# Performance work log

Hardware: AMD Instinct MI355X
Metric: run time of the kernel (lower is better)

The kernel has to match this reference:

```python
import jax, jax.numpy as jnp
import numpy as np

H, DK, NHID, L, G = 8, 32, 256, 2, 16
SQRT_DK = float(np.sqrt(DK))
N_IN = (3, 3, 2)  # number of etypes whose dst is word, topic, doc (for mean cross-reducer)


def _seg_softmax_agg(a, val, dst, n):
    # per-destination-node softmax over incoming edges (DGL mailbox softmax), then weighted sum
    m = jax.ops.segment_max(a, dst, num_segments=n)
    m = jnp.where(m < -1e30, 0.0, m)  # empty segments
    ex = jnp.exp(a - m[dst])
    den = jax.ops.segment_sum(ex, dst, num_segments=n)
    w = ex / jnp.maximum(den, 1e-9)[dst]
    return jax.ops.segment_sum(w[..., None] * val, dst, num_segments=n)  # [n,H,DK]


def _forward(word_id, topic_id, g_word, g_topic, g_doc,
             src_ww, dst_ww, src_wd, dst_wd, src_wt, dst_wt, src_td, dst_td, src_tt, dst_tt,
             time_ww, time_wd, time_wt, time_td, y_data,
             word_embeds, topic_embeds, doc_gen, adapt_w, adapt_b,
             time_tab, time_w, time_b,
             kW, kB, qW, qB, vW, vB, aW, aB, skip, ln_g, ln_b,
             pri, attR, msgR, out_w, out_b):
    nd = g_doc.shape[0]
    # initial node features: word via adapt_ws, topic lookup, doc broadcast
    h = [word_embeds[word_id] @ adapt_w + adapt_b,
         topic_embeds[topic_id],
         jnp.tile(doc_gen, (nd, 1))]
    te = lambda t: time_tab[t] @ time_w + time_b  # RelTemporalEncoding: lin(emb(t)) -> [E, DK]
    th_ww, th_wd, th_wt, th_td = te(time_ww), te(time_wd), te(time_wt), te(time_td)
    # etype index order: wt, wd, td, tt, ww, tw, dt, dw ; ntype index: 0=word,1=topic,2=doc
    rels = [(0, 0, 1, src_wt, dst_wt, th_wt), (1, 0, 2, src_wd, dst_wd, th_wd),
            (2, 1, 2, src_td, dst_td, th_td), (3, 1, 1, src_tt, dst_tt, None),
            (4, 0, 0, src_ww, dst_ww, th_ww), (5, 1, 0, dst_wt, src_wt, th_wt),
            (6, 2, 1, dst_td, src_td, th_td), (7, 2, 0, dst_wd, src_wd, th_wd)]
    for li in range(L):
        k = [(h[i] @ kW[li, i] + kB[li, i]).reshape(-1, H, DK) for i in range(3)]
        q = [(h[i] @ qW[li, i] + qB[li, i]).reshape(-1, H, DK) for i in range(3)]
        v = [(h[i] @ vW[li, i] + vB[li, i]).reshape(-1, H, DK) for i in range(3)]
        t = [jnp.zeros((h[i].shape[0], NHID), h[i].dtype) for i in range(3)]
        for (e, s, d, src, dst, th) in rels:
            key = jnp.einsum('ehk,hkl->ehl', k[s][src], attR[li, e])
            a = (q[d][dst] * key).sum(-1) * pri[li, e] / SQRT_DK  # [E,H]
            val = jnp.einsum('ehk,hkl->ehl', v[s][src], msgR[li, e])
            if th is not None:
                val = val + th[:, None, :]  # temporal encoding broadcast over heads
            n = h[d].shape[0]
            he = _seg_softmax_agg(a, val, dst, n)
            t[d] = t[d] + jax.nn.relu(he.reshape(n, NHID))  # relu per etype, then mean
        nh = []
        for i in range(3):
            alpha = jax.nn.sigmoid(skip[li, i])
            trans = (t[i] / N_IN[i]) @ aW[li, i] + aB[li, i]
            out = trans * alpha + h[i] * (1.0 - alpha)
            mu = out.mean(-1, keepdims=True)
            var = ((out - mu) ** 2).mean(-1, keepdims=True)
            nh.append((out - mu) / jnp.sqrt(var + 1e-5) * ln_g[li, i] + ln_b[li, i])
        h = nh
    gmax = lambda x, g: jax.ops.segment_max(x, g, num_segments=G)  # dgl.max_nodes
    gi = jnp.concatenate([gmax(h[2], g_doc), gmax(h[0], g_word), gmax(h[1], g_topic)], -1)
    logits = gi @ out_w + out_b  # [G,1]
    z = logits.reshape(-1)
    loss = jnp.mean(jnp.maximum(z, 0.0) - z * y_data + jnp.log1p(jnp.exp(-jnp.abs(z))))
    return loss, jax.nn.sigmoid(logits)


def setup_inputs():
    key = jax.random.key(0)
    ks = iter(jax.random.split(key, 80))
    nrm = lambda shape, s=0.05: jax.random.normal(next(ks), shape, jnp.float32) * s
    ri = lambda shape, hi: jax.random.randint(next(ks), shape, 0, hi)
    NW, NT, ND = 30000, 2000, 8000
    d = {}
    d['word_id'] = ri((NW,), 15000)
    d['topic_id'] = ri((NT,), 50)
    d['g_word'] = jnp.sort(ri((NW,), G))
    d['g_topic'] = jnp.sort(ri((NT,), G))
    d['g_doc'] = jnp.sort(ri((ND,), G))
    d['src_ww'] = ri((40000,), NW); d['dst_ww'] = ri((40000,), NW); d['time_ww'] = ri((40000,), 7)
    d['src_wd'] = ri((30000,), NW); d['dst_wd'] = ri((30000,), ND); d['time_wd'] = ri((30000,), 7)
    d['src_wt'] = ri((30000,), NW); d['dst_wt'] = ri((30000,), NT); d['time_wt'] = ri((30000,), 7)
    d['src_td'] = ri((25000,), NT); d['dst_td'] = ri((25000,), ND); d['time_td'] = ri((25000,), 7)
    d['src_tt'] = ri((20000,), NT); d['dst_tt'] = ri((20000,), NT)
    d['y_data'] = jax.random.uniform(next(ks), (G,), jnp.float32)
    d['word_embeds'] = nrm((15000, 256))
    d['topic_embeds'] = nrm((50, 256), 0.1)
    d['doc_gen'] = nrm((1, 256), 0.1)
    d['adapt_w'] = nrm((256, 256)); d['adapt_b'] = nrm((256,), 0.01)
    d['time_tab'] = nrm((7, 32), 0.1); d['time_w'] = nrm((32, 32), 0.1); d['time_b'] = nrm((32,), 0.01)
    for nm in ['kW', 'qW', 'vW', 'aW']:
        d[nm] = nrm((L, 3, 256, 256))
    for nm in ['kB', 'qB', 'vB', 'aB']:
        d[nm] = nrm((L, 3, 256), 0.01)
    d['skip'] = jnp.ones((L, 3))
    d['ln_g'] = jnp.ones((L, 3, 256)); d['ln_b'] = jnp.zeros((L, 3, 256))
    d['pri'] = jnp.ones((L, 8, H))
    d['attR'] = nrm((L, 8, H, DK, DK), 0.1)
    d['msgR'] = nrm((L, 8, H, DK, DK), 0.1)
    d['out_w'] = nrm((3 * NHID, 1)); d['out_b'] = jnp.zeros((1,))
    return d


def reference(word_id, topic_id, g_word, g_topic, g_doc,
              src_ww, dst_ww, time_ww, src_wd, dst_wd, time_wd,
              src_wt, dst_wt, time_wt, src_td, dst_td, time_td,
              src_tt, dst_tt, y_data,
              word_embeds, topic_embeds, doc_gen, adapt_w, adapt_b,
              time_tab, time_w, time_b,
              kW, kB, qW, qB, vW, vB, aW, aB, skip, ln_g, ln_b,
              pri, attR, msgR, out_w, out_b):
    return _forward(word_id, topic_id, g_word, g_topic, g_doc,
                    src_ww, dst_ww, src_wd, dst_wd, src_wt, dst_wt, src_td, dst_td, src_tt, dst_tt,
                    time_ww, time_wd, time_wt, time_td, y_data,
                    word_embeds, topic_embeds, doc_gen, adapt_w, adapt_b,
                    time_tab, time_w, time_b,
                    kW, kB, qW, qB, vW, vB, aW, aB, skip, ln_g, ln_b,
                    pri, attR, msgR, out_w, out_b)
```

## Files before the change

kernel.cpp:

```cpp
#include <hip/hip_runtime.h>
#include <hip/hip_bf16.h>
#include <math.h>

#define H 8
#define DK 32
#define NHID 256
#define LNUM 2
#define GNUM 16

typedef float f32x4 __attribute__((ext_vector_type(4)));
typedef short bf16x8 __attribute__((ext_vector_type(8)));
typedef unsigned short u16x8 __attribute__((ext_vector_type(8)));

__device__ __forceinline__ unsigned encf(float f) {
    unsigned u = __float_as_uint(f);
    return (u & 0x80000000u) ? ~u : (u | 0x80000000u);
}
__device__ __forceinline__ float decf(unsigned u) {
    return __uint_as_float((u & 0x80000000u) ? (u ^ 0x80000000u) : ~u);
}
__device__ __forceinline__ float bfd(unsigned short u) {
    return __uint_as_float(((unsigned)u) << 16);
}
__device__ __forceinline__ unsigned short f2bf(float x) {
    __hip_bfloat16 b = __float2bfloat16(x);
    return *reinterpret_cast<unsigned short*>(&b);
}

#define APAN2(row, kb) ((((kb) >> 7) << 12) + ((row) << 6) + ((((kb) & 127) ^ (((row) & 7) << 4)) >> 1))
__device__ __forceinline__ size_t swzA(int row, int col ) {
    return (((size_t)(row >> 6)) << 14) + (size_t)APAN2(row & 63, col * 2);
}
#define SWZB(row, kb)  (((row) << 6) + ((((kb) ^ (((row) & 7) << 4))) >> 1))

struct CsrArgs  { const int* dst[8]; int relOfs[9]; int dstBase[8]; };
struct BdAllArgs{ int rows[8]; int srcOfs[8]; int outOfs[8]; };
struct Ek1AllArgs{ const int* src[8]; const int* dst[8]; int E[8]; int eBase[8];
                   int kOfs[8]; int qOfs[8]; };
struct Ek3AllArgs{ const int* src[8]; const int* tim[8]; int eBase[8]; int dstBase[8];
                   int vOfs[8]; int typeRel[9]; int nrT[3]; int cumN[4]; int tOfs[3];
                   float oScale[3]; };
struct GmaxArgs { const float* hp[3]; const int* grp[3]; int n[3]; int colBase[3]; };
struct GBArgs   { int rb[4]; int nLoc[3]; int li3; };
struct MLArgs   { int rowOfs[4]; int nLoc[3]; int li3; };

__global__ void te_kernel(const float* __restrict__ time_tab, const float* __restrict__ time_w,
                          const float* __restrict__ time_b, float* __restrict__ te7) {
    int t = threadIdx.x >> 5, j = threadIdx.x & 31;
    if (t < 7) {
        float s = time_b[j];
        #pragma unroll
        for (int i = 0; i < 32; ++i) s += time_tab[t * 32 + i] * time_w[i * 32 + j];
        te7[t * 32 + j] = s;
    }
}

__global__ void gather_rows(const float* __restrict__ emb, const int* __restrict__ idx,
                            float* __restrict__ out, unsigned short* __restrict__ outB, int n) {
    int row = blockIdx.x, c = threadIdx.x;
    if (row < n) {
        float v = emb[(size_t)idx[row] * 256 + c];
        out[(size_t)row * 256 + c] = v;
        outB[swzA(row, c)] = f2bf(v);
    }
}

__global__ void bcast_row(const float* __restrict__ src, float* __restrict__ out,
                          unsigned short* __restrict__ outB, int n) {
    int row = blockIdx.x, c = threadIdx.x;
    if (row < n) {
        float v = src[c];
        out[(size_t)row * 256 + c] = v;
        outB[swzA(row, c)] = f2bf(v);
    }
}

__global__ __launch_bounds__(256) void wtr_kernel(
    const float* __restrict__ adaptW, const float* __restrict__ kW, const float* __restrict__ qW,
    const float* __restrict__ vW, const float* __restrict__ aW, unsigned short* __restrict__ WT) {
    int z = blockIdx.z;
    const float* src;
    if (z == 0) src = adaptW;
    else if (z < 7)  src = kW + (size_t)(z - 1) * 65536;
    else if (z < 13) src = qW + (size_t)(z - 7) * 65536;
    else if (z < 19) src = vW + (size_t)(z - 13) * 65536;
    else             src = aW + (size_t)(z - 19) * 65536;
    unsigned short* dst = WT + (size_t)z * 65536;
    __shared__ float tile[32][33];
    int tx = threadIdx.x & 31, ty = threadIdx.x >> 5;
    int kb = blockIdx.x * 32, cb = blockIdx.y * 32;
    #pragma unroll
    for (int i = 0; i < 4; ++i)
        tile[ty + i * 8][tx] = src[(size_t)(kb + ty + i * 8) * 256 + cb + tx];
    __syncthreads();
    #pragma unroll
    for (int i = 0; i < 4; ++i) {
        int col = cb + ty + i * 8, k = kb + tx;
        dst[((col >> 6) * 4 + (k >> 6)) * 4096 + SWZB(col & 63, (k & 63) * 2)] =
            f2bf(tile[tx][ty + i * 8]);
    }
}

__global__ __launch_bounds__(256) void gemm_batch(
    const unsigned short* __restrict__ Apan,
    const unsigned short* __restrict__ WT, int wBase, int nz,
    const float* __restrict__ b0, const float* __restrict__ b1, const float* __restrict__ b2,
    void* __restrict__ o0, void* __restrict__ o1, void* __restrict__ o2,
    int outBf16, GBArgs ga)
{
    __shared__ unsigned short As[64 * 256];
    __shared__ unsigned short Bs[2][4096];
    const int tid = threadIdx.x;
    const int lane = tid & 63, wv = tid >> 6;
    const int b = blockIdx.x;
    const int t = (b >= ga.rb[2]) ? 2 : ((b >= ga.rb[1]) ? 1 : 0);
    const int nLoc = ga.nLoc[t];
    const int locRowBase = (b - ga.rb[t]) * 64;
    const int cb6 = blockIdx.y;
    const int mBase = wBase + ga.li3 + t;
    {
        const u16x8* src = reinterpret_cast<const u16x8*>(Apan + (((size_t)b) << 14));
        u16x8* dst = reinterpret_cast<u16x8*>(As);
        #pragma unroll
        for (int it = 0; it < 8; ++it)
            dst[it * 256 + tid] = src[it * 256 + tid];
    }
    const int fr = lane & 15, fg = lane >> 4;
    const int wrow = (wv & 1) * 32, wcol = (wv >> 1) * 32;
    const int nt = nz * 4;
    {
        const u16x8* src = reinterpret_cast<const u16x8*>(WT + (size_t)mBase * 65536 + (size_t)(cb6 * 4 + 0) * 4096);
        u16x8* dst = reinterpret_cast<u16x8*>(Bs[0]);
        dst[tid] = src[tid];
        dst[tid + 256] = src[tid + 256];
    }
    __syncthreads();

    f32x4 acc[2][2];
    #pragma unroll
    for (int m = 0; m < 2; ++m)
        #pragma unroll
        for (int nn = 0; nn < 2; ++nn) acc[m][nn] = 0.f;

    for (int tt2 = 0; tt2 < nt; ++tt2) {
        const int cur = tt2 & 1;
        const int ks = tt2 & 3, z = tt2 >> 2;
        u16x8 w0, w1;
        const bool pf = (tt2 + 1 < nt);
        if (pf) {
            int tn = tt2 + 1;
            const u16x8* src = reinterpret_cast<const u16x8*>(
                WT + (size_t)(mBase + (tn >> 2) * 6) * 65536 + (size_t)(cb6 * 4 + (tn & 3)) * 4096);
            w0 = src[tid];
            w1 = src[tid + 256];
        }
        #pragma unroll
        for (int kk = 0; kk < 2; ++kk) {
            bf16x8 af0 = *reinterpret_cast<bf16x8*>(&As[APAN2(wrow + fr,      ks * 128 + kk * 64 + fg * 16)]);
            bf16x8 af1 = *reinterpret_cast<bf16x8*>(&As[APAN2(wrow + 16 + fr, ks * 128 + kk * 64 + fg * 16)]);
            bf16x8 bf0 = *reinterpret_cast<bf16x8*>(&Bs[cur][SWZB(wcol + fr,      kk * 64 + fg * 16)]);
            bf16x8 bf1 = *reinterpret_cast<bf16x8*>(&Bs[cur][SWZB(wcol + 16 + fr, kk * 64 + fg * 16)]);
            acc[0][0] = __builtin_amdgcn_mfma_f32_16x16x32_bf16(af0, bf0, acc[0][0], 0, 0, 0);
            acc[0][1] = __builtin_amdgcn_mfma_f32_16x16x32_bf16(af0, bf1, acc[0][1], 0, 0, 0);
            acc[1][0] = __builtin_amdgcn_mfma_f32_16x16x32_bf16(af1, bf0, acc[1][0], 0, 0, 0);
            acc[1][1] = __builtin_amdgcn_mfma_f32_16x16x32_bf16(af1, bf1, acc[1][1], 0, 0, 0);
        }
        if (pf) {
            u16x8* dst = reinterpret_cast<u16x8*>(Bs[cur ^ 1]);
            dst[tid] = w0;
            dst[tid + 256] = w1;
        }
        if (ks == 3) {
            const float* biasB = (z == 0) ? b0 : ((z == 1) ? b1 : b2);
            const float* bias = biasB + (size_t)(ga.li3 + t) * 256;
            void* outp = (z == 0) ? o0 : ((z == 1) ? o1 : o2);
            #pragma unroll
            for (int m = 0; m < 2; ++m) {
                #pragma unroll
                for (int r = 0; r < 4; ++r) {
                    int lr = locRowBase + wrow + m * 16 + fg * 4 + r;
                    if (lr >= nLoc) continue;
                    size_t gr = (size_t)b * 64 + wrow + m * 16 + fg * 4 + r;
                    #pragma unroll
                    for (int nn = 0; nn < 2; ++nn) {
                        int gc = cb6 * 64 + wcol + nn * 16 + fr;
                        float v = acc[m][nn][r] + bias[gc];
                        if (outBf16) ((unsigned short*)outp)[gr * 256 + gc] = f2bf(v);
                        else         ((float*)outp)[gr * 256 + gc] = v;
                    }
                }
            }
            #pragma unroll
            for (int m = 0; m < 2; ++m)
                #pragma unroll
                for (int nn = 0; nn < 2; ++nn) acc[m][nn] = 0.f;
        }
        __syncthreads();
    }
}

__global__ __launch_bounds__(256) void gemm_init(
    const float* __restrict__ A, const int* __restrict__ gidx,
    const unsigned short* __restrict__ WT, const float* __restrict__ bias,
    float* __restrict__ outF, unsigned short* __restrict__ dupB, int n)
{
    __shared__ unsigned short As[64 * 256];
    __shared__ unsigned short Bs[2][4096];
    const int tid = threadIdx.x;
    const int lane = tid & 63, wv = tid >> 6;
    const int rowBase = blockIdx.x * 64;
    const int cb6 = blockIdx.y;
    #pragma unroll 4
    for (int it = 0; it < 16; ++it) {
        int row = it * 4 + wv;
        int r = rowBase + row;
        ushort4 p = make_ushort4(0, 0, 0, 0);
        if (r < n) {
            int ar = gidx[r];
            float4 v = *reinterpret_cast<const float4*>(A + (size_t)ar * 256 + lane * 4);
            p.x = f2bf(v.x); p.y = f2bf(v.y); p.z = f2bf(v.z); p.w = f2bf(v.w);
        }
        *reinterpret_cast<ushort4*>(&As[APAN2(row, lane * 8)]) = p;
    }
    const int fr = lane & 15, fg = lane >> 4;
    const int wrow = (wv & 1) * 32, wcol = (wv >> 1) * 32;
    {
        const u16x8* src = reinterpret_cast<const u16x8*>(WT + (size_t)(cb6 * 4 + 0) * 4096);
        u16x8* dst = reinterpret_cast<u16x8*>(Bs[0]);
        dst[tid] = src[tid];
        dst[tid + 256] = src[tid + 256];
    }
    __syncthreads();
    f32x4 acc[2][2];
    #pragma unroll
    for (int m = 0; m < 2; ++m)
        #pragma unroll
        for (int nn = 0; nn < 2; ++nn) acc[m][nn] = 0.f;
    for (int t = 0; t < 4; ++t) {
        const int cur = t & 1;
        u16x8 w0, w1;
        const bool pf = (t + 1 < 4);
        if (pf) {
            const u16x8* src = reinterpret_cast<const u16x8*>(WT + (size_t)(cb6 * 4 + t + 1) * 4096);
            w0 = src[tid];
            w1 = src[tid + 256];
        }
        #pragma unroll
        for (int kk = 0; kk < 2; ++kk) {
            bf16x8 af0 = *reinterpret_cast<bf16x8*>(&As[APAN2(wrow + fr,      t * 128 + kk * 64 + fg * 16)]);
            bf16x8 af1 = *reinterpret_cast<bf16x8*>(&As[APAN2(wrow + 16 + fr, t * 128 + kk * 64 + fg * 16)]);
            bf16x8 bf0 = *reinterpret_cast<bf16x8*>(&Bs[cur][SWZB(wcol + fr,      kk * 64 + fg * 16)]);
            bf16x8 bf1 = *reinterpret_cast<bf16x8*>(&Bs[cur][SWZB(wcol + 16 + fr, kk * 64 + fg * 16)]);
            acc[0][0] = __builtin_amdgcn_mfma_f32_16x16x32_bf16(af0, bf0, acc[0][0], 0, 0, 0);
            acc[0][1] = __builtin_amdgcn_mfma_f32_16x16x32_bf16(af0, bf1, acc[0][1], 0, 0, 0);
            acc[1][0] = __builtin_amdgcn_mfma_f32_16x16x32_bf16(af1, bf0, acc[1][0], 0, 0, 0);
            acc[1][1] = __builtin_amdgcn_mfma_f32_16x16x32_bf16(af1, bf1, acc[1][1], 0, 0, 0);
        }
        if (pf) {
            u16x8* dst = reinterpret_cast<u16x8*>(Bs[cur ^ 1]);
            dst[tid] = w0;
            dst[tid + 256] = w1;
        }
        __syncthreads();
    }
    #pragma unroll
    for (int m = 0; m < 2; ++m) {
        #pragma unroll
        for (int r = 0; r < 4; ++r) {
            int gr = rowBase + wrow + m * 16 + fg * 4 + r;
            if (gr >= n) continue;
            #pragma unroll
            for (int nn = 0; nn < 2; ++nn) {
                int gc = cb6 * 64 + wcol + nn * 16 + fr;
                float v = acc[m][nn][r] + bias[gc];
                outF[(size_t)gr * 256 + gc] = v;
                dupB[swzA(gr, gc)] = f2bf(v);
            }
        }
    }
}

__global__ __launch_bounds__(256) void bd_all(
    const unsigned short* __restrict__ inPb, const float* __restrict__ Rl,
    const float* __restrict__ priL, int isV,
    unsigned short* __restrict__ outAll, BdAllArgs A)
{
    const int rel = blockIdx.z;
    const int n = A.rows[rel];
    const int rowBase = blockIdx.x * 128;
    if (rowBase >= n) return;
    const unsigned short* in = inPb + (size_t)A.srcOfs[rel] * 256;
    const float* R = Rl + (size_t)rel * 8192;
    unsigned short* out = outAll + (size_t)A.outOfs[rel] * 256;
    const int head = blockIdx.y;
    const float oscale = isV ? 1.f : (priL[rel * 8 + head] * 0.17677669529663687f);
    const int tid = threadIdx.x, lane = tid & 63, wv = tid >> 6;
    const int fr = lane & 15, fg = lane >> 4;
    const float* Rh = R + head * 1024;
    bf16x8 b0, b1;
    #pragma unroll
    for (int j = 0; j < 8; ++j) {
        b0[j] = (short)f2bf(Rh[(fg * 8 + j) * 32 + fr] * oscale);
        b1[j] = (short)f2bf(Rh[(fg * 8 + j) * 32 + 16 + fr] * oscale);
    }
    const int r0 = rowBase + wv * 32 + fr;
    const int r1 = r0 + 16;
    const int rc0 = (r0 < n) ? r0 : n - 1;
    const int rc1 = (r1 < n) ? r1 : n - 1;
    bf16x8 a0 = *reinterpret_cast<const bf16x8*>(in + (size_t)rc0 * 256 + head * 32 + fg * 8);
    bf16x8 a1 = *reinterpret_cast<const bf16x8*>(in + (size_t)rc1 * 256 + head * 32 + fg * 8);
    f32x4 acc00 = 0.f, acc01 = 0.f, acc10 = 0.f, acc11 = 0.f;
    acc00 = __builtin_amdgcn_mfma_f32_16x16x32_bf16(a0, b0, acc00, 0, 0, 0);
    acc01 = __builtin_amdgcn_mfma_f32_16x16x32_bf16(a0, b1, acc01, 0, 0, 0);
    acc10 = __builtin_amdgcn_mfma_f32_16x16x32_bf16(a1, b0, acc10, 0, 0, 0);
    acc11 = __builtin_amdgcn_mfma_f32_16x16x32_bf16(a1, b1, acc11, 0, 0, 0);
    const int colB = head * 32 + fr;
    #pragma unroll
    for (int r = 0; r < 4; ++r) {
        int g0 = rowBase + wv * 32 + fg * 4 + r;
        if (g0 < n) {
            out[(size_t)g0 * 256 + colB]      = f2bf(acc00[r]);
            out[(size_t)g0 * 256 + colB + 16] = f2bf(acc01[r]);
        }
        int g1 = g0 + 16;
        if (g1 < n) {
            out[(size_t)g1 * 256 + colB]      = f2bf(acc10[r]);
            out[(size_t)g1 * 256 + colB + 16] = f2bf(acc11[r]);
        }
    }
}

__global__ __launch_bounds__(256) void ek1_all(
    const unsigned short* __restrict__ qPb, const unsigned short* __restrict__ kattAll,
    float* __restrict__ alog, Ek1AllArgs A)
{
    const int rel = blockIdx.y;
    int gid = blockIdx.x * 256 + threadIdx.x;
    int e = gid >> 3, h = gid & 7;
    if (e >= A.E[rel]) return;
    int s = A.src[rel][e], d = A.dst[rel][e];
    const u16x8* q8 = reinterpret_cast<const u16x8*>(qPb + ((size_t)(A.qOfs[rel] + d)) * 256 + h * 32);
    const u16x8* k8 = reinterpret_cast<const u16x8*>(kattAll + ((size_t)(A.kOfs[rel] + s)) * 256 + h * 32);
    float a = 0.f;
    #pragma unroll
    for (int j = 0; j < 4; ++j) {
        u16x8 qv = q8[j], kv = k8[j];
        #pragma unroll
        for (int m = 0; m < 8; ++m) a += bfd(qv[m]) * bfd(kv[m]);
    }
    alog[(size_t)(A.eBase[rel] + e) * 8 + h] = a;
}

__global__ __launch_bounds__(256) void ek3_all(
    const unsigned short* __restrict__ vmsgAll, const float* __restrict__ alog,
    const int* __restrict__ rowptrAll, const int* __restrict__ eidxAll,
    const float* __restrict__ te7, unsigned short* __restrict__ tB, Ek3AllArgs A)
{
    __shared__ float sTe[224];
    if (threadIdx.x < 224) sTe[threadIdx.x] = te7[threadIdx.x];
    __syncthreads();
    int wv = threadIdx.x >> 6, lane = threadIdx.x & 63;
    int dg = blockIdx.x * 4 + wv;
    if (dg >= A.cumN[3]) return;
    const int ty = (dg >= A.cumN[2]) ? 2 : ((dg >= A.cumN[1]) ? 1 : 0);
    const int d = dg - A.cumN[ty];
    const int bl = lane >> 3, hl = lane & 7;
    const int c = lane * 4, hq = lane >> 3;
    float t0 = 0.f, t1 = 0.f, t2 = 0.f, t3 = 0.f;
    const int nr = A.nrT[ty];
    for (int j = 0; j < nr; ++j) {
        const int rel = A.typeRel[ty * 3 + j];
        int base = A.dstBase[rel] + d;
        int beg = rowptrAll[base], end = rowptrAll[base + 1];
        if (beg == end) continue;
        const int* srcp = A.src[rel];
        const int* timp = A.tim[rel];
        int eB = A.eBase[rel], rO = A.vOfs[rel];
        float m = -INFINITY, den = 0.f;
        float a0 = 0.f, a1 = 0.f, a2 = 0.f, a3 = 0.f;
        for (int p0 = beg; p0 < end; p0 += 8) {
            int p = p0 + bl;
            bool valid = p < end;
            int ge = eidxAll[valid ? p : end - 1];
            int le = ge - eB;
            float a = valid ? alog[(size_t)ge * 8 + hl] : -INFINITY;
            int sS = valid ? srcp[le] : 0;
            int tT = (timp && valid) ? timp[le] : 0;
            float bm = a;
            bm = fmaxf(bm, __shfl_xor(bm, 8));
            bm = fmaxf(bm, __shfl_xor(bm, 16));
            bm = fmaxf(bm, __shfl_xor(bm, 32));
            float bmA = __shfl(bm, hq);
            float mN = fmaxf(m, bmA);
            float sc = __expf(m - mN);
            den *= sc; a0 *= sc; a1 *= sc; a2 *= sc; a3 *= sc;
            m = mN;
            float mL = __shfl(mN, hl * 8);
            float ex = valid ? __expf(a - mL) : 0.f;
            float ds = ex;
            ds += __shfl_xor(ds, 8);
            ds += __shfl_xor(ds, 16);
            ds += __shfl_xor(ds, 32);
            den += __shfl(ds, hq);
            int nb = end - p0; if (nb > 8) nb = 8;
            for (int b = 0; b < nb; ++b) {
                float w = __shfl(ex, b * 8 + hq);
                int sB = __shfl(sS, b * 8);
                ushort4 v = *reinterpret_cast<const ushort4*>(vmsgAll + ((size_t)(rO + sB)) * 256 + c);
                float vx = bfd(v.x), vy = bfd(v.y), vz = bfd(v.z), vw = bfd(v.w);
                if (timp) {
                    int tBt = __shfl(tT, b * 8);
                    const float* tp = &sTe[tBt * 32 + (c & 31)];
                    vx += tp[0]; vy += tp[1]; vz += tp[2]; vw += tp[3];
                }
                a0 += w * vx; a1 += w * vy; a2 += w * vz; a3 += w * vw;
            }
        }
        float inv = 1.f / fmaxf(den, 1e-9f);
        t0 += fmaxf(a0 * inv, 0.f); t1 += fmaxf(a1 * inv, 0.f);
        t2 += fmaxf(a2 * inv, 0.f); t3 += fmaxf(a3 * inv, 0.f);
    }
    float os = A.oScale[ty];
    ushort4 o;
    o.x = f2bf(t0 * os); o.y = f2bf(t1 * os);
    o.z = f2bf(t2 * os); o.w = f2bf(t3 * os);
    *reinterpret_cast<ushort4*>(tB + swzA(A.tOfs[ty] + d, c)) = o;
}

__global__ void count_all(CsrArgs A, int* __restrict__ cnt, int totE) {
    int gid = blockIdx.x * 256 + threadIdx.x;
    if (gid >= totE) return;
    int r = 0;
    while (gid >= A.relOfs[r + 1]) ++r;
    int e = gid - A.relOfs[r];
    atomicAdd(&cnt[A.dstBase[r] + A.dst[r][e]], 1);
}
__global__ __launch_bounds__(1024) void scan1_k(const int* __restrict__ cnt, int* __restrict__ part,
                                                int* __restrict__ bsum, int n) {
    __shared__ int buf[1024];
    int tid = threadIdx.x, gid = blockIdx.x * 1024 + tid;
    int x = (gid < n) ? cnt[gid] : 0;
    buf[tid] = x; __syncthreads();
    for (int off = 1; off < 1024; off <<= 1) {
        int y = (tid >= off) ? buf[tid - off] : 0;
        __syncthreads();
        buf[tid] += y;
        __syncthreads();
    }
    if (gid < n) part[gid] = buf[tid];
    if (tid == 1023) bsum[blockIdx.x] = buf[1023];
}
__global__ __launch_bounds__(256) void scan2_k(int* __restrict__ bsum, int nb) {
    __shared__ int buf[256];
    int tid = threadIdx.x;
    buf[tid] = (tid < nb) ? bsum[tid] : 0;
    __syncthreads();
    for (int off = 1; off < 256; off <<= 1) {
        int y = (tid >= off) ? buf[tid - off] : 0;
        __syncthreads();
        buf[tid] += y;
        __syncthreads();
    }
    if (tid < nb) bsum[tid] = buf[tid];
}
__global__ void scan3_k(const int* __restrict__ cnt, const int* __restrict__ part,
                        const int* __restrict__ bsum, int* __restrict__ rowptr,
                        int* __restrict__ cur, int n) {
    int gid = blockIdx.x * 256 + threadIdx.x;
    if (gid < n) {
        int b = gid >> 10;
        int add = (b > 0) ? bsum[b - 1] : 0;
        int inc = part[gid] + add;
        rowptr[gid + 1] = inc;
        cur[gid] = inc - cnt[gid];
    }
    if (gid == 0) rowptr[0] = 0;
}
__global__ void scatter_all(CsrArgs A, int* __restrict__ cur, int* __restrict__ eidx, int totE) {
    int gid = blockIdx.x * 256 + threadIdx.x;
    if (gid >= totE) return;
    int r = 0;
    while (gid >= A.relOfs[r + 1]) ++r;
    int e = gid - A.relOfs[r];
    int p = atomicAdd(&cur[A.dstBase[r] + A.dst[r][e]], 1);
    eidx[p] = gid;
}

__global__ __launch_bounds__(256) void mix_ln_all(
    float* __restrict__ h, unsigned short* __restrict__ hB, const float* __restrict__ trans,
    const float* __restrict__ skipP, const float* __restrict__ g, const float* __restrict__ b,
    MLArgs M)
{
    int row = blockIdx.x;
    int t = (row >= M.rowOfs[2]) ? 2 : ((row >= M.rowOfs[1]) ? 1 : 0);
    int d = row - M.rowOfs[t];
    if (d >= M.nLoc[t]) return;
    int j = M.li3 + t;
    int c = threadIdx.x;
    float alpha = 1.f / (1.f + expf(-skipP[j]));
    size_t off = (size_t)row * 256 + c;
    float o = trans[off] * alpha + h[off] * (1.f - alpha);
    float s = o, ss = o * o;
    #pragma unroll
    for (int dd = 1; dd < 64; dd <<= 1) { s += __shfl_xor(s, dd); ss += __shfl_xor(ss, dd); }
    __shared__ float rS[4], rSS[4];
    int w = threadIdx.x >> 6, lane = threadIdx.x & 63;
    if (lane == 0) { rS[w] = s; rSS[w] = ss; }
    __syncthreads();
    float S = rS[0] + rS[1] + rS[2] + rS[3];
    float SS = rSS[0] + rSS[1] + rSS[2] + rSS[3];
    float mean = S * (1.f / 256.f);
    float var = fmaxf(SS * (1.f / 256.f) - mean * mean, 0.f);
    float rs = rsqrtf(var + 1e-5f);
    float v = (o - mean) * rs * g[(size_t)j * 256 + c] + b[(size_t)j * 256 + c];
    h[off] = v;
    hB[swzA(row, c)] = f2bf(v);
}

__global__ __launch_bounds__(256) void gmax_all(GmaxArgs A, unsigned* __restrict__ gi) {
    int ty = blockIdx.y;
    int n = A.n[ty];
    int r0 = blockIdx.x * 64;
    if (r0 >= n) return;
    int col = threadIdx.x;
    const float* hp = A.hp[ty];
    const int* grp = A.grp[ty];
    int cbase = A.colBase[ty];
    int rend = (r0 + 64 < n) ? r0 + 64 : n;
    int cur = grp[r0];
    float m = -INFINITY;
    for (int r = r0; r < rend; ++r) {
        int g = grp[r];
        if (g != cur) {
            atomicMax(&gi[cur * 768 + cbase + col], encf(m));
            cur = g; m = -INFINITY;
        }
        m = fmaxf(m, hp[(size_t)r * 256 + col]);
    }
    atomicMax(&gi[cur * 768 + cbase + col], encf(m));
}

__global__ void gi_init(unsigned* __restrict__ gi) {
    int i = blockIdx.x * 256 + threadIdx.x;
    if (i < 16 * 768) gi[i] = 0x007FFFFFu;
}

__global__ __launch_bounds__(1024) void final_k(const unsigned* __restrict__ gi,
                                                const float* __restrict__ out_w,
                                                const float* __restrict__ out_b,
                                                const float* __restrict__ y,
                                                float* __restrict__ out) {
    int w = threadIdx.x >> 6, lane = threadIdx.x & 63;
    float s = 0.f;
    for (int c = lane; c < 768; c += 64) s += decf(gi[w * 768 + c]) * out_w[c];
    #pragma unroll
    for (int d = 1; d < 64; d <<= 1) s += __shfl_xor(s, d);
    __shared__ float lloss[16];
    if (lane == 0) {
        float z = s + out_b[0];
        out[1 + w] = 1.f / (1.f + expf(-z));
        lloss[w] = fmaxf(z, 0.f) - z * y[w] + log1pf(expf(-fabsf(z)));
    }
    __syncthreads();
    if (threadIdx.x == 0) {
        float L = 0.f;
        for (int g2 = 0; g2 < 16; ++g2) L += lloss[g2];
        out[0] = L * (1.f / 16.f);
    }
}

extern "C" void kernel_launch(void* const* d_in, const int* in_sizes, int n_in,
                              void* d_out, int out_size, void* d_ws, size_t ws_size,
                              hipStream_t stream) {
    const int* word_id   = (const int*)d_in[0];
    const int* topic_id  = (const int*)d_in[1];
    const int* g_word    = (const int*)d_in[2];
    const int* g_topic   = (const int*)d_in[3];
    const int* g_doc     = (const int*)d_in[4];
    const int* src_ww = (const int*)d_in[5];  const int* dst_ww = (const int*)d_in[6];  const int* time_ww = (const int*)d_in[7];
    const int* src_wd = (const int*)d_in[8];  const int* dst_wd = (const int*)d_in[9];  const int* time_wd = (const int*)d_in[10];
    const int* src_wt = (const int*)d_in[11]; const int* dst_wt = (const int*)d_in[12]; const int* time_wt = (const int*)d_in[13];
    const int* src_td = (const int*)d_in[14]; const int* dst_td = (const int*)d_in[15]; const int* time_td = (const int*)d_in[16];
    const int* src_tt = (const int*)d_in[17]; const int* dst_tt = (const int*)d_in[18];
    const float* y_data      = (const float*)d_in[19];
    const float* word_embeds = (const float*)d_in[20];
    const float* topic_embeds= (const float*)d_in[21];
    const float* doc_gen     = (const float*)d_in[22];
    const float* adapt_w     = (const float*)d_in[23];
    const float* adapt_b     = (const float*)d_in[24];
    const float* time_tab    = (const float*)d_in[25];
    const float* time_w      = (const float*)d_in[26];
    const float* time_b      = (const float*)d_in[27];
    const float* kW = (const float*)d_in[28];
    const float* qW = (const float*)d_in[29];
    const float* vW = (const float*)d_in[30];
    const float* aW = (const float*)d_in[31];
    const float* kB = (const float*)d_in[32];
    const float* qB = (const float*)d_in[33];
    const float* vB = (const float*)d_in[34];
    const float* aB = (const float*)d_in[35];
    const float* skip = (const float*)d_in[36];
    const float* ln_g = (const float*)d_in[37];
    const float* ln_b = (const float*)d_in[38];
    const float* pri  = (const float*)d_in[39];
    const float* attR = (const float*)d_in[40];
    const float* msgR = (const float*)d_in[41];
    const float* out_w = (const float*)d_in[42];
    const float* out_b = (const float*)d_in[43];

    const int NW = in_sizes[0], NT = in_sizes[1], ND = in_sizes[4];
    const int E_ww = in_sizes[5], E_wd = in_sizes[8], E_wt = in_sizes[11],
              E_td = in_sizes[14], E_tt = in_sizes[17];
    const int nN[3] = {NW, NT, ND};
    const float invNin[3] = {1.f / 3.f, 1.f / 3.f, 1.f / 2.f};

    struct Rel { int e, s, d; const int* src; const int* dst; const int* tim; int E; };
    const Rel rels[8] = {
        {0, 0, 1, src_wt, dst_wt, time_wt, E_wt},
        {1, 0, 2, src_wd, dst_wd, time_wd, E_wd},
        {2, 1, 2, src_td, dst_td, time_td, E_td},
        {3, 1, 1, src_tt, dst_tt, nullptr, E_tt},
        {4, 0, 0, src_ww, dst_ww, time_ww, E_ww},
        {5, 1, 0, dst_wt, src_wt, time_wt, E_wt},
        {6, 2, 1, dst_td, src_td, time_td, E_td},
        {7, 2, 0, dst_wd, src_wd, time_wd, E_wd},
    };

    int relOfs[9]; relOfs[0] = 0;
    int dstBase[8]; int acc = 0;
    for (int r = 0; r < 8; ++r) { relOfs[r + 1] = relOfs[r] + rels[r].E; dstBase[r] = acc; acc += nN[rels[r].d]; }
    const int totE = relOfs[8], totD = acc;

    int relRowOfs[8], relRowsTot = 0, maxRelRows = 0, maxE = 0;
    for (int r = 0; r < 8; ++r) {
        relRowOfs[r] = relRowsTot;
        relRowsTot += nN[rels[r].s];
        if (nN[rels[r].s] > maxRelRows) maxRelRows = nN[rels[r].s];
        if (rels[r].E > maxE) maxE = rels[r].E;
    }

    int nPad[3], rowOfsT[4];
    rowOfsT[0] = 0;
    for (int i = 0; i < 3; ++i) { nPad[i] = (nN[i] + 63) & ~63; rowOfsT[i + 1] = rowOfsT[i] + nPad[i]; }
    const int totPad = rowOfsT[3];

    float* base = (float*)d_ws;
    size_t off = 0;
    auto take = [&](size_t nElems) { float* p = base + off; off += (nElems + 63) & ~(size_t)63; return p; };
    float* hPbase = take((size_t)totPad * 256);
    unsigned short* hB = (unsigned short*)take((size_t)totPad * 128);
    unsigned short* tB = (unsigned short*)take((size_t)totPad * 128);
    unsigned short* kPb = (unsigned short*)take((size_t)totPad * 128);
    unsigned short* qPb = (unsigned short*)take((size_t)totPad * 128);
    unsigned short* vPb = (unsigned short*)take((size_t)totPad * 128);
    size_t arenaFloats = (size_t)relRowsTot * 128;
    if ((size_t)totPad * 256 > arenaFloats) arenaFloats = (size_t)totPad * 256;
    float* uni = take(arenaFloats);
    unsigned short* arena = (unsigned short*)uni;
    float* trans = uni;
    unsigned short* WT = (unsigned short*)take((size_t)25 * 32768);
    float* alog = take((size_t)totE * 8);
    float* te7  = take(7 * 32);
    unsigned* gi = (unsigned*)take(16 * 768);
    int* cntAll = (int*)take(totD);
    int* part   = (int*)take(totD);
    int* bsum   = (int*)take(256);
    int* rowptrAll = (int*)take(totD + 1);
    int* curAll = (int*)take(totD);
    int* eidxAll = (int*)take(totE);
    (void)ws_size; (void)n_in; (void)out_size;

    te_kernel<<<1, 256, 0, stream>>>(time_tab, time_w, time_b, te7);
    {
        dim3 g(8, 8, 25);
        wtr_kernel<<<g, 256, 0, stream>>>(adapt_w, kW, qW, vW, aW, WT);
    }
    CsrArgs ca;
    for (int r = 0; r < 8; ++r) { ca.dst[r] = rels[r].dst; ca.dstBase[r] = dstBase[r]; }
    for (int r = 0; r < 9; ++r) ca.relOfs[r] = relOfs[r];
    hipMemsetAsync(cntAll, 0, (size_t)totD * sizeof(int), stream);
    count_all<<<(totE + 255) / 256, 256, 0, stream>>>(ca, cntAll, totE);
    int nb = (totD + 1023) / 1024;
    scan1_k<<<nb, 1024, 0, stream>>>(cntAll, part, bsum, totD);
    scan2_k<<<1, 256, 0, stream>>>(bsum, nb);
    scan3_k<<<(totD + 255) / 256, 256, 0, stream>>>(cntAll, part, bsum, rowptrAll, curAll, totD);
    scatter_all<<<(totE + 255) / 256, 256, 0, stream>>>(ca, curAll, eidxAll, totE);
    gi_init<<<48, 256, 0, stream>>>(gi);

    {
        dim3 g((NW + 63) / 64, 4);
        gemm_init<<<g, 256, 0, stream>>>(word_embeds, word_id, WT, adapt_b, hPbase, hB, NW);
    }
    gather_rows<<<NT, 256, 0, stream>>>(topic_embeds, topic_id,
                                        hPbase + (size_t)rowOfsT[1] * 256,
                                        hB + (size_t)rowOfsT[1] * 256, NT);
    bcast_row<<<ND, 256, 0, stream>>>(doc_gen,
                                      hPbase + (size_t)rowOfsT[2] * 256,
                                      hB + (size_t)rowOfsT[2] * 256, ND);

    BdAllArgs ba;
    Ek1AllArgs e1;
    Ek3AllArgs e3;
    for (int r = 0; r < 8; ++r) {
        const Rel& R = rels[r];
        ba.rows[r] = nN[R.s];
        ba.srcOfs[r] = rowOfsT[R.s];
        ba.outOfs[r] = relRowOfs[r];
        e1.src[r] = R.src; e1.dst[r] = R.dst; e1.E[r] = R.E; e1.eBase[r] = relOfs[r];
        e1.kOfs[r] = relRowOfs[r]; e1.qOfs[r] = rowOfsT[R.d];
        e3.src[r] = R.src; e3.tim[r] = R.tim; e3.eBase[r] = relOfs[r];
        e3.dstBase[r] = dstBase[r]; e3.vOfs[r] = relRowOfs[r];
    }
    const int typeRel[9] = {4, 5, 7, 0, 3, 6, 1, 2, 0};
    for (int i = 0; i < 9; ++i) e3.typeRel[i] = typeRel[i];
    e3.nrT[0] = 3; e3.nrT[1] = 3; e3.nrT[2] = 2;
    e3.cumN[0] = 0; e3.cumN[1] = NW; e3.cumN[2] = NW + NT; e3.cumN[3] = NW + NT + ND;
    for (int i = 0; i < 3; ++i) { e3.tOfs[i] = rowOfsT[i]; e3.oScale[i] = invNin[i]; }

    GBArgs gb;
    for (int i = 0; i < 4; ++i) gb.rb[i] = rowOfsT[i] / 64;
    for (int i = 0; i < 3; ++i) gb.nLoc[i] = nN[i];
    MLArgs ml;
    for (int i = 0; i < 4; ++i) ml.rowOfs[i] = rowOfsT[i];
    for (int i = 0; i < 3; ++i) ml.nLoc[i] = nN[i];

    const int totBlocks = totPad / 64;
    const int totD3 = NW + NT + ND;
    for (int li = 0; li < LNUM; ++li) {
        gb.li3 = li * 3; ml.li3 = li * 3;
        {
            dim3 g(totBlocks, 4);
            gemm_batch<<<g, 256, 0, stream>>>(hB, WT, 1, 3, kB, qB, vB,
                                              kPb, qPb, vPb, 1, gb);
        }
        {
            dim3 g((maxRelRows + 127) / 128, 8, 8);
            bd_all<<<g, 256, 0, stream>>>(kPb, attR + (size_t)li * 8 * 8192,
                                          pri + (size_t)li * 8 * 8, 0, arena, ba);
        }
        {
            dim3 g((maxE * 8 + 255) / 256, 8);
            ek1_all<<<g, 256, 0, stream>>>(qPb, arena, alog, e1);
        }
        {
            dim3 g((maxRelRows + 127) / 128, 8, 8);
            bd_all<<<g, 256, 0, stream>>>(vPb, msgR + (size_t)li * 8 * 8192,
                                          pri + (size_t)li * 8 * 8, 1, arena, ba);
        }
        ek3_all<<<(totD3 + 3) / 4, 256, 0, stream>>>(arena, alog, rowptrAll, eidxAll,
                                                     te7, tB, e3);
        {
            dim3 g(totBlocks, 4);
            gemm_batch<<<g, 256, 0, stream>>>(tB, WT, 19, 1, aB, aB, aB,
                                              trans, trans, trans, 0, gb);
        }
        mix_ln_all<<<totPad, 256, 0, stream>>>(hPbase, hB, trans, skip, ln_g, ln_b, ml);
    }

    GmaxArgs ga;
    ga.hp[0] = hPbase + (size_t)rowOfsT[2] * 256; ga.grp[0] = g_doc;   ga.n[0] = ND; ga.colBase[0] = 0;
    ga.hp[1] = hPbase;                             ga.grp[1] = g_word;  ga.n[1] = NW; ga.colBase[1] = 256;
    ga.hp[2] = hPbase + (size_t)rowOfsT[1] * 256; ga.grp[2] = g_topic; ga.n[2] = NT; ga.colBase[2] = 512;
    int maxN = NW > ND ? (NW > NT ? NW : NT) : (ND > NT ? ND : NT);
    dim3 gg((maxN + 63) / 64, 3);
    gmax_all<<<gg, 256, 0, stream>>>(ga, gi);
    final_k<<<1, 1024, 0, stream>>>(gi, out_w, out_b, y_data, (float*)d_out);
}
```

Measured before the change: 676.4 us.

## Store edge data in CSR order with packed src/time payload

The scatter step now writes each edge's source and time index into one packed int, and its destination and relation into a second, both in CSR position order, instead of writing a global edge index. ek1 runs over CSR positions and writes logits contiguously, so ek3 reads logits and payload sequentially rather than through eidx and per-relation src/tim indirection. This cuts dependent gathers in the aggregation kernel and improves locality of the q-row reads in ek1. In exchange, ek1 issues scattered k-row reads, and the packing assumes source ids fit in 16 bits and destination ids in 20 bits.

```diff
diff --git a/kernel.cpp b/kernel.cpp
--- a/kernel.cpp
+++ b/kernel.cpp
@@ -33,13 +33,12 @@
 }
 #define SWZB(row, kb)  (((row) << 6) + ((((kb) ^ (((row) & 7) << 4))) >> 1))
 
-struct CsrArgs  { const int* dst[8]; int relOfs[9]; int dstBase[8]; };
+struct CsrArgs  { const int* dst[8]; const int* srcA[8]; const int* timA[8];
+                  int relOfs[9]; int dstBase[8]; };
 struct BdAllArgs{ int rows[8]; int srcOfs[8]; int outOfs[8]; };
-struct Ek1AllArgs{ const int* src[8]; const int* dst[8]; int E[8]; int eBase[8];
-                   int kOfs[8]; int qOfs[8]; };
-struct Ek3AllArgs{ const int* src[8]; const int* tim[8]; int eBase[8]; int dstBase[8];
-                   int vOfs[8]; int typeRel[9]; int nrT[3]; int cumN[4]; int tOfs[3];
-                   float oScale[3]; };
+struct Ek1PosArgs{ int kOfs[8]; int qOfs[8]; };
+struct Ek3AllArgs{ int dstBase[8]; int vOfs[8]; int hasTim[8]; int typeRel[9]; int nrT[3];
+                   int cumN[4]; int tOfs[3]; float oScale[3]; };
 struct GmaxArgs { const float* hp[3]; const int* grp[3]; int n[3]; int colBase[3]; };
 struct GBArgs   { int rb[4]; int nLoc[3]; int li3; };
 struct MLArgs   { int rowOfs[4]; int nLoc[3]; int li3; };
@@ -330,15 +329,17 @@
     }
 }
 
-__global__ __launch_bounds__(256) void ek1_all(
+__global__ __launch_bounds__(256) void ek1_pos(
     const unsigned short* __restrict__ qPb, const unsigned short* __restrict__ kattAll,
-    float* __restrict__ alog, Ek1AllArgs A)
+    const int* __restrict__ payload, const int* __restrict__ drel,
+    float* __restrict__ alogC, Ek1PosArgs A, int totE)
 {
-    const int rel = blockIdx.y;
     int gid = blockIdx.x * 256 + threadIdx.x;
-    int e = gid >> 3, h = gid & 7;
-    if (e >= A.E[rel]) return;
-    int s = A.src[rel][e], d = A.dst[rel][e];
+    int p = gid >> 3, h = gid & 7;
+    if (p >= totE) return;
+    int dr = drel[p];
+    int d = dr & 0xFFFFF, rel = dr >> 20;
+    int s = payload[p] & 0xFFFF;
     const u16x8* q8 = reinterpret_cast<const u16x8*>(qPb + ((size_t)(A.qOfs[rel] + d)) * 256 + h * 32);
     const u16x8* k8 = reinterpret_cast<const u16x8*>(kattAll + ((size_t)(A.kOfs[rel] + s)) * 256 + h * 32);
     float a = 0.f;
@@ -348,12 +349,12 @@
         #pragma unroll
         for (int m = 0; m < 8; ++m) a += bfd(qv[m]) * bfd(kv[m]);
     }
-    alog[(size_t)(A.eBase[rel] + e) * 8 + h] = a;
+    alogC[(size_t)p * 8 + h] = a;
 }
 
 __global__ __launch_bounds__(256) void ek3_all(
-    const unsigned short* __restrict__ vmsgAll, const float* __restrict__ alog,
-    const int* __restrict__ rowptrAll, const int* __restrict__ eidxAll,
+    const unsigned short* __restrict__ vmsgAll, const float* __restrict__ alogC,
+    const int* __restrict__ rowptrAll, const int* __restrict__ payload,
     const float* __restrict__ te7, unsigned short* __restrict__ tB, Ek3AllArgs A)
 {
     __shared__ float sTe[224];
@@ -373,19 +374,17 @@
         int base = A.dstBase[rel] + d;
         int beg = rowptrAll[base], end = rowptrAll[base + 1];
         if (beg == end) continue;
-        const int* srcp = A.src[rel];
-        const int* timp = A.tim[rel];
-        int eB = A.eBase[rel], rO = A.vOfs[rel];
+        const int useTim = A.hasTim[rel];
+        int rO = A.vOfs[rel];
         float m = -INFINITY, den = 0.f;
         float a0 = 0.f, a1 = 0.f, a2 = 0.f, a3 = 0.f;
         for (int p0 = beg; p0 < end; p0 += 8) {
             int p = p0 + bl;
             bool valid = p < end;
-            int ge = eidxAll[valid ? p : end - 1];
-            int le = ge - eB;
-            float a = valid ? alog[(size_t)ge * 8 + hl] : -INFINITY;
-            int sS = valid ? srcp[le] : 0;
-            int tT = (timp && valid) ? timp[le] : 0;
+            int pc = valid ? p : end - 1;
+            float a = valid ? alogC[(size_t)pc * 8 + hl] : -INFINITY;
+            int pk = payload[pc];
+            int sS = pk & 0xFFFF, tT = pk >> 16;
             float bm = a;
             bm = fmaxf(bm, __shfl_xor(bm, 8));
             bm = fmaxf(bm, __shfl_xor(bm, 16));
@@ -408,7 +407,7 @@
                 int sB = __shfl(sS, b * 8);
                 ushort4 v = *reinterpret_cast<const ushort4*>(vmsgAll + ((size_t)(rO + sB)) * 256 + c);
                 float vx = bfd(v.x), vy = bfd(v.y), vz = bfd(v.z), vw = bfd(v.w);
-                if (timp) {
+                if (useTim) {
                     int tBt = __shfl(tT, b * 8);
                     const float* tp = &sTe[tBt * 32 + (c & 31)];
                     vx += tp[0]; vy += tp[1]; vz += tp[2]; vw += tp[3];
@@ -476,14 +475,19 @@
     }
     if (gid == 0) rowptr[0] = 0;
 }
-__global__ void scatter_all(CsrArgs A, int* __restrict__ cur, int* __restrict__ eidx, int totE) {
+__global__ void scatter_all(CsrArgs A, int* __restrict__ cur,
+                            int* __restrict__ payload, int* __restrict__ drel, int totE) {
     int gid = blockIdx.x * 256 + threadIdx.x;
     if (gid >= totE) return;
     int r = 0;
     while (gid >= A.relOfs[r + 1]) ++r;
     int e = gid - A.relOfs[r];
-    int p = atomicAdd(&cur[A.dstBase[r] + A.dst[r][e]], 1);
-    eidx[p] = gid;
+    int d = A.dst[r][e];
+    int p = atomicAdd(&cur[A.dstBase[r] + d], 1);
+    int s = A.srcA[r][e];
+    int t = A.timA[r] ? A.timA[r][e] : 0;
+    payload[p] = s | (t << 16);
+    drel[p] = d | (r << 20);
 }
 
 __global__ __launch_bounds__(256) void mix_ln_all(
@@ -631,12 +635,11 @@
     for (int r = 0; r < 8; ++r) { relOfs[r + 1] = relOfs[r] + rels[r].E; dstBase[r] = acc; acc += nN[rels[r].d]; }
     const int totE = relOfs[8], totD = acc;
 
-    int relRowOfs[8], relRowsTot = 0, maxRelRows = 0, maxE = 0;
+    int relRowOfs[8], relRowsTot = 0, maxRelRows = 0;
     for (int r = 0; r < 8; ++r) {
         relRowOfs[r] = relRowsTot;
         relRowsTot += nN[rels[r].s];
         if (nN[rels[r].s] > maxRelRows) maxRelRows = nN[rels[r].s];
-        if (rels[r].E > maxE) maxE = rels[r].E;
     }
 
     int nPad[3], rowOfsT[4];
@@ -659,7 +662,7 @@
     unsigned short* arena = (unsigned short*)uni;
     float* trans = uni;
     unsigned short* WT = (unsigned short*)take((size_t)25 * 32768);
-    float* alog = take((size_t)totE * 8);
+    float* alogC = take((size_t)totE * 8);
     float* te7  = take(7 * 32);
     unsigned* gi = (unsigned*)take(16 * 768);
     int* cntAll = (int*)take(totD);
@@ -667,7 +670,8 @@
     int* bsum   = (int*)take(256);
     int* rowptrAll = (int*)take(totD + 1);
     int* curAll = (int*)take(totD);
-    int* eidxAll = (int*)take(totE);
+    int* payload = (int*)take(totE);
+    int* drel    = (int*)take(totE);
     (void)ws_size; (void)n_in; (void)out_size;
 
     te_kernel<<<1, 256, 0, stream>>>(time_tab, time_w, time_b, te7);
@@ -676,7 +680,10 @@
         wtr_kernel<<<g, 256, 0, stream>>>(adapt_w, kW, qW, vW, aW, WT);
     }
     CsrArgs ca;
-    for (int r = 0; r < 8; ++r) { ca.dst[r] = rels[r].dst; ca.dstBase[r] = dstBase[r]; }
+    for (int r = 0; r < 8; ++r) {
+        ca.dst[r] = rels[r].dst; ca.srcA[r] = rels[r].src; ca.timA[r] = rels[r].tim;
+        ca.dstBase[r] = dstBase[r];
+    }
     for (int r = 0; r < 9; ++r) ca.relOfs[r] = relOfs[r];
     hipMemsetAsync(cntAll, 0, (size_t)totD * sizeof(int), stream);
     count_all<<<(totE + 255) / 256, 256, 0, stream>>>(ca, cntAll, totE);
@@ -684,7 +691,7 @@
     scan1_k<<<nb, 1024, 0, stream>>>(cntAll, part, bsum, totD);
     scan2_k<<<1, 256, 0, stream>>>(bsum, nb);
     scan3_k<<<(totD + 255) / 256, 256, 0, stream>>>(cntAll, part, bsum, rowptrAll, curAll, totD);
-    scatter_all<<<(totE + 255) / 256, 256, 0, stream>>>(ca, curAll, eidxAll, totE);
+    scatter_all<<<(totE + 255) / 256, 256, 0, stream>>>(ca, curAll, payload, drel, totE);
     gi_init<<<48, 256, 0, stream>>>(gi);
 
     {
@@ -699,17 +706,16 @@
                                       hB + (size_t)rowOfsT[2] * 256, ND);
 
     BdAllArgs ba;
-    Ek1AllArgs e1;
+    Ek1PosArgs e1;
     Ek3AllArgs e3;
     for (int r = 0; r < 8; ++r) {
         const Rel& R = rels[r];
         ba.rows[r] = nN[R.s];
         ba.srcOfs[r] = rowOfsT[R.s];
         ba.outOfs[r] = relRowOfs[r];
-        e1.src[r] = R.src; e1.dst[r] = R.dst; e1.E[r] = R.E; e1.eBase[r] = relOfs[r];
         e1.kOfs[r] = relRowOfs[r]; e1.qOfs[r] = rowOfsT[R.d];
-        e3.src[r] = R.src; e3.tim[r] = R.tim; e3.eBase[r] = relOfs[r];
         e3.dstBase[r] = dstBase[r]; e3.vOfs[r] = relRowOfs[r];
+        e3.hasTim[r] = (R.tim != nullptr) ? 1 : 0;
     }
     const int typeRel[9] = {4, 5, 7, 0, 3, 6, 1, 2, 0};
     for (int i = 0; i < 9; ++i) e3.typeRel[i] = typeRel[i];
@@ -738,16 +744,14 @@
             bd_all<<<g, 256, 0, stream>>>(kPb, attR + (size_t)li * 8 * 8192,
                                           pri + (size_t)li * 8 * 8, 0, arena, ba);
         }
-        {
-            dim3 g((maxE * 8 + 255) / 256, 8);
-            ek1_all<<<g, 256, 0, stream>>>(qPb, arena, alog, e1);
-        }
+        ek1_pos<<<((size_t)totE * 8 + 255) / 256, 256, 0, stream>>>(
+            qPb, arena, payload, drel, alogC, e1, totE);
         {
             dim3 g((maxRelRows + 127) / 128, 8, 8);
             bd_all<<<g, 256, 0, stream>>>(vPb, msgR + (size_t)li * 8 * 8192,
                                           pri + (size_t)li * 8 * 8, 1, arena, ba);
         }
-        ek3_all<<<(totD3 + 3) / 4, 256, 0, stream>>>(arena, alog, rowptrAll, eidxAll,
+        ek3_all<<<(totD3 + 3) / 4, 256, 0, stream>>>(arena, alogC, rowptrAll, payload,
                                                      te7, tB, e3);
         {
             dim3 g(totBlocks, 4);
```

After: 658.2 us, median of 2. 1.03x faster.
